# Kernel tuning notes

Hardware: AMD Instinct MI355X
Metric: run time of the kernel (lower is better)

## Reference

```python
import jax, jax.numpy as jnp
import numpy as np

EPS = 1e-5
N_HEADS = 4

def _ln(x, s, b):
    m = x.mean(-1, keepdims=True)
    v = ((x - m) ** 2).mean(-1, keepdims=True)
    return (x - m) / jnp.sqrt(v + EPS) * s + b

def _gelu(x):
    return jax.nn.gelu(x, approximate=False)  # torch nn.GELU default (erf)


def setup_inputs() -> dict:
    key = jax.random.key(0)
    ks = jax.random.split(key, 20)
    H, AF, BF, DEPTH = 256, 153, 14, 4
    n_mols, apm = 1024, 48
    n_atoms = n_mols * apm          # 49152
    max_nb = 6
    n_bonds = 3 * n_atoms           # 147456 directed bonds
    def nrm(k, shape, scale=0.02):
        return jax.random.normal(k, shape, jnp.float32) * scale
    return dict(
        f_atoms=jax.random.normal(ks[0], (n_atoms, AF), jnp.float32),
        f_bonds=jax.random.normal(ks[1], (n_bonds, BF), jnp.float32),
        a2b=jax.random.randint(ks[2], (n_atoms, max_nb), 0, n_bonds),
        b2a=jax.random.randint(ks[3], (n_bonds,), 0, n_atoms),
        b2revb=jax.random.randint(ks[4], (n_bonds,), 0, n_bonds),
        W_i=nrm(ks[5], (AF + BF, H)), b_i=jnp.zeros((H,), jnp.float32),
        W_h=nrm(ks[6], (DEPTH - 1, H, H)), b_h=jnp.zeros((DEPTH - 1, H), jnp.float32),
        ln_msg_s=jnp.ones((DEPTH - 1, H), jnp.float32), ln_msg_b=jnp.zeros((DEPTH - 1, H), jnp.float32),
        W_o=nrm(ks[7], (AF + H, H)), b_o=jnp.zeros((H,), jnp.float32),
        ln_atom_s=jnp.ones((H,), jnp.float32), ln_atom_b=jnp.zeros((H,), jnp.float32),
        q_w=nrm(ks[8], (H, H)), q_b=jnp.zeros((H,), jnp.float32),
        k_w=nrm(ks[9], (H, H)), k_b=jnp.zeros((H,), jnp.float32),
        v_w=nrm(ks[10], (H, H)), v_b=jnp.zeros((H,), jnp.float32),
        o_w=nrm(ks[11], (H, H)), o_b=jnp.zeros((H,), jnp.float32),
        ln1_s=jnp.ones((H,), jnp.float32), ln1_b=jnp.zeros((H,), jnp.float32),
        ln2_s=jnp.ones((H,), jnp.float32), ln2_b=jnp.zeros((H,), jnp.float32),
        ff1_w=nrm(ks[12], (H, 2 * H)), ff1_b=jnp.zeros((2 * H,), jnp.float32),
        ff2_w=nrm(ks[13], (2 * H, H)), ff2_b=jnp.zeros((H,), jnp.float32),
        readout_query=nrm(ks[14], (1, 1, H)),
        rk_w=nrm(ks[15], (H, H)), rk_b=jnp.zeros((H,), jnp.float32),
        n_mols=n_mols, atoms_per_mol=apm,
    )


def reference(f_atoms, f_bonds, a2b, b2a, b2revb,
              W_i, b_i, W_h, b_h, ln_msg_s, ln_msg_b, W_o, b_o,
              ln_atom_s, ln_atom_b, q_w, q_b, k_w, k_b, v_w, v_b, o_w, o_b,
              ln1_s, ln1_b, ln2_s, ln2_b, ff1_w, ff1_b, ff2_w, ff2_b,
              readout_query, rk_w, rk_b, n_mols, atoms_per_mol):
    H = W_i.shape[1]
    HD = H // N_HEADS
    depth = W_h.shape[0] + 1

    # ---- D-MPNN message passing over directed bonds ----
    message = _gelu(jnp.concatenate([f_atoms[b2a], f_bonds], axis=1) @ W_i + b_i)  # [n_bonds,H]
    for t in range(depth - 1):  # fixed small depth loop
        nei = message[a2b].sum(axis=1)                 # [n_atoms,H] gather-sum over incoming bonds
        nei_m = nei[b2a] - message[b2revb]             # [n_bonds,H] subtract reverse bond
        message = message + _gelu(_ln(nei_m, ln_msg_s[t], ln_msg_b[t]) @ W_h[t] + b_h[t])

    a_message = message[a2b].sum(axis=1)               # [n_atoms,H]
    atom_h = _gelu(jnp.concatenate([f_atoms, a_message], axis=1) @ W_o + b_o)
    atom_h = _ln(atom_h, ln_atom_s, ln_atom_b)

    # uniform scopes: padding loop becomes a reshape, mask is all-valid
    x = atom_h.reshape(n_mols, atoms_per_mol, H)

    # ---- pre-norm TransformerEncoderLayer ----
    h = _ln(x, ln1_s, ln1_b)
    def heads(t):
        return t.reshape(n_mols, atoms_per_mol, N_HEADS, HD).transpose(0, 2, 1, 3)
    q = heads(h @ q_w + q_b)
    k = heads(h @ k_w + k_b)
    v = heads(h @ v_w + v_b)
    attn = jax.nn.softmax(jnp.einsum('bhqd,bhkd->bhqk', q, k) / float(np.sqrt(HD)), axis=-1)
    ctx = jnp.einsum('bhqk,bhkd->bhqd', attn, v).transpose(0, 2, 1, 3).reshape(n_mols, atoms_per_mol, H)
    x = x + (ctx @ o_w + o_b)
    h2 = _ln(x, ln2_s, ln2_b)
    x = x + (_gelu(h2 @ ff1_w + ff1_b) @ ff2_w + ff2_b)

    # ---- attention-weighted readout ----
    keys = x @ rk_w + rk_b                             # [B,S,H]
    scores = jnp.einsum('bsh,h->bs', keys, readout_query[0, 0])
    w = jax.nn.softmax(scores, axis=-1)[..., None]
    return (x * w).sum(axis=1)                         # [B,H]
```

## Files before the change

### kernel.cpp

```cpp
#include <hip/hip_runtime.h>
#include <hip/hip_bf16.h>
#include <math.h>

#define H 256
#define AFEAT 153
#define BFEAT 14
#define KINIT 167
#define NA 49152
#define NB 147456
#define NMOL 1024
#define APM 48
#define MAXNB 6
#define NHEAD 4
#define HDIM 64
#define EPSLN 1e-5f
#define KI_PAD 192
#define KO_PAD 448

typedef unsigned short u16;
typedef __attribute__((ext_vector_type(8))) short bf16x8;
typedef __attribute__((ext_vector_type(4))) short bf16x4;
typedef __attribute__((ext_vector_type(4))) float f32x4;

__device__ __forceinline__ float gelu_f(float x) {
    float t = -1.5957691216f * x * (1.0f + 0.044715f * x * x);
    float e = __expf(t);
#if __has_builtin(__builtin_amdgcn_rcpf)
    return x * __builtin_amdgcn_rcpf(1.0f + e);
#else
    return x / (1.0f + e);
#endif
}
__device__ __forceinline__ float wave_sum(float v) {
    #pragma unroll
    for (int m = 1; m < 64; m <<= 1) v += __shfl_xor(v, m);
    return v;
}
__device__ __forceinline__ float b2f(u16 u) {
    union { unsigned u32; float f; } c; c.u32 = ((unsigned)u) << 16; return c.f;
}
__device__ __forceinline__ float blo(unsigned w) {
    union { unsigned u; float f; } c; c.u = w << 16; return c.f;
}
__device__ __forceinline__ float bhi(unsigned w) {
    union { unsigned u; float f; } c; c.u = w & 0xffff0000u; return c.f;
}
__device__ __forceinline__ u16 f2b(float f) {
    __hip_bfloat16 h = __float2bfloat16(f);
    u16 u; __builtin_memcpy(&u, &h, 2); return u;
}
__device__ __forceinline__ ushort4 f2b4(float a, float b, float c, float d) {
    ushort4 o; o.x = f2b(a); o.y = f2b(b); o.z = f2b(c); o.w = f2b(d); return o;
}
__device__ __forceinline__ void up8(uint4 u, float* v) {
    v[0]=blo(u.x); v[1]=bhi(u.x); v[2]=blo(u.y); v[3]=bhi(u.y);
    v[4]=blo(u.z); v[5]=bhi(u.z); v[6]=blo(u.w); v[7]=bhi(u.w);
}
__device__ __forceinline__ unsigned addbf2(unsigned a, unsigned b) {
    float lo = b2f((u16)(a & 0xffff)) + b2f((u16)(b & 0xffff));
    float hi = b2f((u16)(a >> 16)) + b2f((u16)(b >> 16));
    return ((unsigned)f2b(hi) << 16) | (unsigned)f2b(lo);
}
__device__ __forceinline__ uint4 addbf8(uint4 a, uint4 b) {
    uint4 r;
    r.x = addbf2(a.x, b.x); r.y = addbf2(a.y, b.y);
    r.z = addbf2(a.z, b.z); r.w = addbf2(a.w, b.w);
    return r;
}

__device__ __forceinline__ f32x4 mfma16(bf16x4 a, bf16x4 b, f32x4 c) {
#if __has_builtin(__builtin_amdgcn_mfma_f32_16x16x16bf16_1k)
    return __builtin_amdgcn_mfma_f32_16x16x16bf16_1k(a, b, c, 0, 0, 0);
#elif __has_builtin(__builtin_amdgcn_mfma_f32_16x16x16_bf16_1k)
    return __builtin_amdgcn_mfma_f32_16x16x16_bf16_1k(a, b, c, 0, 0, 0);
#elif __has_builtin(__builtin_amdgcn_mfma_f32_16x16x16_bf16)
    return __builtin_amdgcn_mfma_f32_16x16x16_bf16(a, b, c, 0, 0, 0);
#else
    f32x4 d;
    asm("v_mfma_f32_16x16x16_bf16 %0, %1, %2, %3"
        : "=&v"(d) : "v"(a), "v"(b), "v"(c));
    return d;
#endif
}

typedef const __attribute__((address_space(1))) void* gas_ptr;
typedef __attribute__((address_space(3))) void* las_ptr;
__device__ __forceinline__ void gload_lds16(const u16* g, u16* l) {
    __builtin_amdgcn_global_load_lds((gas_ptr)g, (las_ptr)l, 16, 0, 0);
}

template<bool GELU, bool ACCUM>
__global__ __launch_bounds__(256) void gemm_mfma_k(
    const u16* __restrict__ A, int Ka,
    const u16* __restrict__ Wt,
    const float* __restrict__ bias,
    u16* __restrict__ C, int Nc, int K)
{
    __shared__ __align__(16) u16 S[128 * 128];
    u16* As = S;
    u16* Bs = S + 8192;
    const int tid = threadIdx.x;
    const int w = tid >> 6, l = tid & 63;
    const int r0 = blockIdx.x * 128;
    const int cb0 = blockIdx.y * 128;
    const int wr = (w >> 1) * 64;
    const int wc = (w & 1) * 64;

    f32x4 acc[4][4];
    #pragma unroll
    for (int m = 0; m < 4; ++m)
        #pragma unroll
        for (int n = 0; n < 4; ++n) acc[m][n] = (f32x4){0.f, 0.f, 0.f, 0.f};

    const int srow = l >> 3;
    const int ssrc = ((l & 7) * 16) ^ (srow << 4);
    const int fr = l & 15;
    const int fh = l >> 4;
    const int swz = (fr & 7) << 4;

    for (int k0 = 0; k0 < K; k0 += 64) {
        #pragma unroll
        for (int i = 0; i < 4; ++i) {
            const int seg = w * 4 + i;
            gload_lds16(A + (size_t)(r0 + seg * 8 + srow) * Ka + k0 + (ssrc >> 1),
                        &As[seg * 512]);
            gload_lds16(Wt + (size_t)(cb0 + seg * 8 + srow) * Ka + k0 + (ssrc >> 1),
                        &Bs[seg * 512]);
        }
        __syncthreads();
        #pragma unroll
        for (int s = 0; s < 2; ++s) {
            const int cbyte = ((s * 64 + fh * 16) ^ swz) >> 1;
            bf16x8 af[4], bv[4];
            #pragma unroll
            for (int m = 0; m < 4; ++m)
                af[m] = *(const bf16x8*)&As[(wr + m * 16 + fr) * 64 + cbyte];
            #pragma unroll
            for (int n = 0; n < 4; ++n)
                bv[n] = *(const bf16x8*)&Bs[(wc + n * 16 + fr) * 64 + cbyte];
            #pragma unroll
            for (int m = 0; m < 4; ++m)
                #pragma unroll
                for (int n = 0; n < 4; ++n)
                    acc[m][n] = __builtin_amdgcn_mfma_f32_16x16x32_bf16(
                        af[m], bv[n], acc[m][n], 0, 0, 0);
        }
        __syncthreads();
    }

    float bvv[4];
    #pragma unroll
    for (int n = 0; n < 4; ++n) bvv[n] = bias[cb0 + wc + n * 16 + fr];
    #pragma unroll
    for (int m = 0; m < 4; ++m)
        #pragma unroll
        for (int n = 0; n < 4; ++n) {
            const int col = wc + n * 16 + fr;
            #pragma unroll
            for (int j = 0; j < 4; ++j) {
                const int row = wr + m * 16 + fh * 4 + j;
                float v = acc[m][n][j] + bvv[n];
                if (GELU) v = gelu_f(v);
                *(u16*)((char*)S + row * 256 + ((col * 2) ^ ((row & 7) << 4))) = f2b(v);
            }
        }
    __syncthreads();
    {
        const int rrow = tid >> 1;
        const int rch = (tid & 1) * 128;
        const int rswz = (rrow & 7) << 4;
        u16* gp = C + (size_t)(r0 + rrow) * Nc + cb0 + (tid & 1) * 64;
        #pragma unroll
        for (int q = 0; q < 8; ++q) {
            uint4 dv = *(const uint4*)((const char*)S + rrow * 256 + ((rch + q * 16) ^ rswz));
            if (ACCUM) {
                uint4 ov = *(const uint4*)(gp + q * 8);
                dv = addbf8(dv, ov);
            }
            *(uint4*)(gp + q * 8) = dv;
        }
    }
}

struct LGather {
    const u16* nei; const u16* msg; const int* b2a; const int* b2revb;
    __device__ __forceinline__ void load16(int row, int g, float* v) const {
        const int a = b2a[row], rv = b2revb[row];
        const uint4* np = (const uint4*)(nei + (size_t)a * H + g * 16);
        const uint4* mp = (const uint4*)(msg + (size_t)rv * H + g * 16);
        float nv[16], mv[16];
        up8(np[0], nv); up8(np[1], nv + 8);
        up8(mp[0], mv); up8(mp[1], mv + 8);
        #pragma unroll
        for (int j = 0; j < 16; ++j) v[j] = nv[j] - mv[j];
    }
};
struct LPlain {
    const u16* X;
    __device__ __forceinline__ void load16(int row, int g, float* v) const {
        const uint4* p = (const uint4*)(X + (size_t)row * H + g * 16);
        up8(p[0], v); up8(p[1], v + 8);
    }
};

template<class L, bool GELU, bool ACCUM>
__global__ __launch_bounds__(512, 4) void fln_gemm_k(
    L ld, const u16* __restrict__ Wt,
    const float* __restrict__ lns, const float* __restrict__ lnb,
    const float* __restrict__ bias,
    const u16* __restrict__ Cold,
    u16* __restrict__ C, int Nc)
{
    __shared__ __align__(16) u16 SH[64 * 256 + 2 * 256 * 32];
    u16* Alds = SH;
    u16* Bbuf0 = SH + 16384;
    u16* Bbuf1 = SH + 16384 + 8192;
    const int tid = threadIdx.x;
    const int w = tid >> 6, l = tid & 63;
    const int r0 = blockIdx.x * 64;
    const int cb0 = blockIdx.y * 256;
    const int fr = l & 15, fh = l >> 4;
    const int swzf = (fr & 7) << 4;

    uint4 oldv[4];
    if (ACCUM) {
        const u16* op = Cold + (size_t)(r0 + (tid >> 3)) * Nc + cb0 + (tid & 7) * 32;
        #pragma unroll
        for (int q = 0; q < 4; ++q) oldv[q] = *(const uint4*)(op + q * 8);
    }

    #define STAGE_B(BB, KK) do {                                               \
        _Pragma("unroll")                                                      \
        for (int j_ = 0; j_ < 2; ++j_) {                                       \
            const int seg_ = w * 2 + j_;                                       \
            const int n_ = seg_ * 16 + (l >> 2);                               \
            const int u_ = (n_ & 3) ^ ((n_ >> 2) & 3);                         \
            gload_lds16(Wt + (size_t)(cb0 + n_) * H + (KK) * 32                \
                        + (((l & 3) ^ u_) << 3), (BB) + seg_ * 512);           \
        }                                                                      \
    } while (0)
    STAGE_B(Bbuf0, 0);

    {
        const int g = l & 15;
        float4 sv[4], bb[4];
        #pragma unroll
        for (int q = 0; q < 4; ++q) {
            sv[q] = *(const float4*)(lns + g * 16 + q * 4);
            bb[q] = *(const float4*)(lnb + g * 16 + q * 4);
        }
        #pragma unroll
        for (int i = 0; i < 2; ++i) {
            const int r = w * 8 + i * 4 + (l >> 4);
            float v[16];
            ld.load16(r0 + r, g, v);
            float s = 0.f, s2 = 0.f;
            #pragma unroll
            for (int j = 0; j < 16; ++j) { s += v[j]; s2 = fmaf(v[j], v[j], s2); }
            #pragma unroll
            for (int m = 1; m < 16; m <<= 1) {
                s += __shfl_xor(s, m);
                s2 += __shfl_xor(s2, m);
            }
            const float mean = s * (1.0f / H);
            const float var = fmaxf(s2 * (1.0f / H) - mean * mean, 0.f);
            const float inv = rsqrtf(var + EPSLN);
            const int swr = (r & 7) << 4;
            #pragma unroll
            for (int q = 0; q < 4; ++q) {
                const float* sq = (const float*)&sv[q];
                const float* bq = (const float*)&bb[q];
                ushort4 o = f2b4((v[q*4+0]-mean)*inv*sq[0] + bq[0],
                                 (v[q*4+1]-mean)*inv*sq[1] + bq[1],
                                 (v[q*4+2]-mean)*inv*sq[2] + bq[2],
                                 (v[q*4+3]-mean)*inv*sq[3] + bq[3]);
                *(ushort4*)((char*)Alds + r * 512 + ((g * 32 + q * 8) ^ swr)) = o;
            }
        }
    }

    f32x4 acc[2][4];
    #pragma unroll
    for (int m = 0; m < 2; ++m)
        #pragma unroll
        for (int n = 0; n < 4; ++n) acc[m][n] = (f32x4){0.f, 0.f, 0.f, 0.f};

    const int wr = (w >> 2) * 32;
    const int wc = (w & 3) * 64;

    __syncthreads();

    #pragma unroll
    for (int kk = 0; kk < 8; ++kk) {
        if (kk < 7) STAGE_B((kk & 1) ? Bbuf0 : Bbuf1, kk + 1);
        const u16* Bb = (kk & 1) ? Bbuf1 : Bbuf0;
        bf16x8 af[2], bv[4];
        #pragma unroll
        for (int m = 0; m < 2; ++m)
            af[m] = *(const bf16x8*)((const char*)Alds + (wr + m * 16 + fr) * 512
                    + ((kk * 64 + fh * 16) ^ swzf));
        #pragma unroll
        for (int n = 0; n < 4; ++n) {
            const int nc = wc + n * 16 + fr;
            const int u = (nc & 3) ^ ((nc >> 2) & 3);
            bv[n] = *(const bf16x8*)((const char*)Bb + nc * 64 + ((fh ^ u) << 4));
        }
        #pragma unroll
        for (int m = 0; m < 2; ++m)
            #pragma unroll
            for (int n = 0; n < 4; ++n)
                acc[m][n] = __builtin_amdgcn_mfma_f32_16x16x32_bf16(
                    af[m], bv[n], acc[m][n], 0, 0, 0);
        __syncthreads();
    }
    #undef STAGE_B

    float bvv[4];
    #pragma unroll
    for (int n = 0; n < 4; ++n) bvv[n] = bias[cb0 + wc + n * 16 + fr];
    #pragma unroll
    for (int m = 0; m < 2; ++m)
        #pragma unroll
        for (int n = 0; n < 4; ++n) {
            const int col = wc + n * 16 + fr;
            #pragma unroll
            for (int j = 0; j < 4; ++j) {
                const int row = wr + m * 16 + fh * 4 + j;
                float v = acc[m][n][j] + bvv[n];
                if (GELU) v = gelu_f(v);
                *(u16*)((char*)Alds + row * 512 + ((col * 2) ^ ((row & 7) << 4))) = f2b(v);
            }
        }
    __syncthreads();
    {
        const int rrow = tid >> 3;
        const int rch = (tid & 7) * 64;
        const int rswz = (rrow & 7) << 4;
        u16* gp = C + (size_t)(r0 + rrow) * Nc + cb0 + (tid & 7) * 32;
        #pragma unroll
        for (int q = 0; q < 4; ++q) {
            uint4 dv = *(const uint4*)((const char*)Alds + rrow * 512 + ((rch + q * 16) ^ rswz));
            if (ACCUM) dv = addbf8(dv, oldv[q]);
            *(uint4*)(gp + q * 8) = dv;
        }
    }
}

__global__ __launch_bounds__(256) void wcvt_k(const float* __restrict__ W,
    u16* __restrict__ Wt, int K, int N, int Kpad)
{
    int idx = blockIdx.x * 256 + threadIdx.x;
    if (idx >= N * Kpad) return;
    int n = idx / Kpad, kp = idx - n * Kpad;
    Wt[idx] = (kp < K) ? f2b(W[(size_t)kp * N + n]) : (u16)0;
}

__global__ void biaspack_k(const float* q, const float* k, const float* v, float* dst) {
    int t = threadIdx.x;
    dst[t] = q[t]; dst[256 + t] = k[t]; dst[512 + t] = v[t];
}

__global__ __launch_bounds__(256) void ainit_k(const float* __restrict__ fa,
    const float* __restrict__ fb, const int* __restrict__ b2a, u16* __restrict__ dst)
{
    const int w = threadIdx.x >> 6, l = threadIdx.x & 63;
    const int row = blockIdx.x * 4 + w;
    const int a = b2a[row];
    const float* fsrc = fa + (size_t)a * AFEAT;
    u16* d = dst + (size_t)row * KI_PAD;
    #pragma unroll
    for (int i = 0; i < 3; ++i) {
        int c = l + i * 64;
        float v;
        if (c < AFEAT) v = fsrc[c];
        else if (c < KINIT) v = fb[(size_t)row * BFEAT + (c - AFEAT)];
        else v = 0.f;
        d[c] = f2b(v);
    }
}

__global__ __launch_bounds__(256) void acat_k(const float* __restrict__ fa,
    const u16* __restrict__ nei, u16* __restrict__ dst)
{
    const int w = threadIdx.x >> 6, l = threadIdx.x & 63;
    const int row = blockIdx.x * 4 + w;
    const float* fsrc = fa + (size_t)row * AFEAT;
    const u16* nsrc = nei + (size_t)row * H;
    u16* d = dst + (size_t)row * KO_PAD;
    #pragma unroll
    for (int i = 0; i < 7; ++i) {
        int c = l + i * 64;
        u16 v;
        if (c < AFEAT) v = f2b(fsrc[c]);
        else if (c < AFEAT + H) v = nsrc[c - AFEAT];
        else v = 0;
        d[c] = v;
    }
}

__global__ __launch_bounds__(256) void nei_sum_k(const u16* __restrict__ msg,
    const int* __restrict__ a2b, u16* __restrict__ nei)
{
    const int wave = threadIdx.x >> 6;
    const int lane = threadIdx.x & 63;
    const int atom = blockIdx.x * 4 + wave;
    float ax = 0.f, ay = 0.f, az = 0.f, aw = 0.f;
    #pragma unroll
    for (int j = 0; j < MAXNB; ++j) {
        int b = a2b[atom * MAXNB + j];
        ushort4 v = *(const ushort4*)(msg + (size_t)b * H + lane * 4);
        ax += b2f(v.x); ay += b2f(v.y); az += b2f(v.z); aw += b2f(v.w);
    }
    *(ushort4*)(nei + (size_t)atom * H + lane * 4) = f2b4(ax, ay, az, aw);
}

__global__ __launch_bounds__(256) void row_ln_k(const u16* __restrict__ in,
    u16* __restrict__ out, const float* __restrict__ s, const float* __restrict__ b)
{
    const int wave = threadIdx.x >> 6;
    const int lane = threadIdx.x & 63;
    const int row = blockIdx.x * 4 + wave;
    ushort4 u = *(const ushort4*)(in + (size_t)row * H + lane * 4);
    float vx = b2f(u.x), vy = b2f(u.y), vz = b2f(u.z), vw = b2f(u.w);
    float mean = wave_sum(vx + vy + vz + vw) * (1.0f / H);
    float dx = vx - mean, dy = vy - mean, dz = vz - mean, dw = vw - mean;
    float var = wave_sum(dx * dx + dy * dy + dz * dz + dw * dw) * (1.0f / H);
    float inv = rsqrtf(var + EPSLN);
    float4 s4 = *(const float4*)(s + lane * 4);
    float4 b4 = *(const float4*)(b + lane * 4);
    *(ushort4*)(out + (size_t)row * H + lane * 4) =
        f2b4(dx * inv * s4.x + b4.x, dy * inv * s4.y + b4.y,
             dz * inv * s4.z + b4.z, dw * inv * s4.w + b4.w);
}

#define VPAD 268
__global__ __launch_bounds__(256) void attn_mfma_k(const u16* __restrict__ qkv,
    u16* __restrict__ ctx)
{
    __shared__ u16 Vs[48][VPAD];
    const int mol = blockIdx.x;
    const int tid = threadIdx.x;
    const int w = tid >> 6;
    const int l = tid & 63;
    const int fr = l & 15;
    const int fh = l >> 4;
    const size_t qb = (size_t)mol * APM * 768;

    {
        const int r = tid >> 4;
        const int c = (tid & 15) * 16;
        #pragma unroll
        for (int i = 0; i < 3; ++i) {
            const int row = r + i * 16;
            const u16* src = qkv + qb + (size_t)row * 768 + 512 + c;
            ushort4 a0 = *(const ushort4*)(src);
            ushort4 a1 = *(const ushort4*)(src + 4);
            ushort4 a2 = *(const ushort4*)(src + 8);
            ushort4 a3 = *(const ushort4*)(src + 12);
            *(ushort4*)&Vs[row][c]      = a0;
            *(ushort4*)&Vs[row][c + 4]  = a1;
            *(ushort4*)&Vs[row][c + 8]  = a2;
            *(ushort4*)&Vs[row][c + 12] = a3;
        }
    }
    __syncthreads();

    f32x4 st[3][3];
    {
        bf16x8 kf[3][2], qf[3][2];
        #pragma unroll
        for (int t = 0; t < 3; ++t)
            #pragma unroll
            for (int ks = 0; ks < 2; ++ks) {
                const size_t rowb = qb + (size_t)(t * 16 + fr) * 768;
                kf[t][ks] = *(const bf16x8*)(qkv + rowb + 256 + w * 64 + ks * 32 + fh * 8);
                qf[t][ks] = *(const bf16x8*)(qkv + rowb +       w * 64 + ks * 32 + fh * 8);
            }
        #pragma unroll
        for (int mi = 0; mi < 3; ++mi)
            #pragma unroll
            for (int ni = 0; ni < 3; ++ni) {
                f32x4 a = (f32x4){0.f, 0.f, 0.f, 0.f};
                a = __builtin_amdgcn_mfma_f32_16x16x32_bf16(kf[mi][0], qf[ni][0], a, 0, 0, 0);
                a = __builtin_amdgcn_mfma_f32_16x16x32_bf16(kf[mi][1], qf[ni][1], a, 0, 0, 0);
                st[mi][ni] = a;
            }
    }

    float inv_sum[3];
    #pragma unroll
    for (int ni = 0; ni < 3; ++ni) {
        float m = -1e30f;
        #pragma unroll
        for (int mi = 0; mi < 3; ++mi)
            #pragma unroll
            for (int j = 0; j < 4; ++j) m = fmaxf(m, st[mi][ni][j]);
        m = fmaxf(m, __shfl_xor(m, 16));
        m = fmaxf(m, __shfl_xor(m, 32));
        float s = 0.f;
        #pragma unroll
        for (int mi = 0; mi < 3; ++mi)
            #pragma unroll
            for (int j = 0; j < 4; ++j) {
                float e = __expf((st[mi][ni][j] - m) * 0.125f);
                st[mi][ni][j] = e;
                s += e;
            }
        s += __shfl_xor(s, 16);
        s += __shfl_xor(s, 32);
        inv_sum[ni] = 1.0f / s;
    }

    bf16x4 pf[3][3];
    #pragma unroll
    for (int mi = 0; mi < 3; ++mi)
        #pragma unroll
        for (int ni = 0; ni < 3; ++ni) {
            bf16x4 p;
            p[0] = (short)f2b(st[mi][ni][0]);
            p[1] = (short)f2b(st[mi][ni][1]);
            p[2] = (short)f2b(st[mi][ni][2]);
            p[3] = (short)f2b(st[mi][ni][3]);
            pf[mi][ni] = p;
        }

    f32x4 co[4][3];
    #pragma unroll
    for (int dt = 0; dt < 4; ++dt)
        #pragma unroll
        for (int ni = 0; ni < 3; ++ni) co[dt][ni] = (f32x4){0.f, 0.f, 0.f, 0.f};
    #pragma unroll
    for (int kt = 0; kt < 3; ++kt) {
        bf16x4 vf[4];
        #pragma unroll
        for (int dt = 0; dt < 4; ++dt) {
            const int colu = w * 64 + dt * 16 + fr;
            bf16x4 t;
            #pragma unroll
            for (int e = 0; e < 4; ++e)
                t[e] = (short)Vs[kt * 16 + fh * 4 + e][colu];
            vf[dt] = t;
        }
        #pragma unroll
        for (int dt = 0; dt < 4; ++dt)
            #pragma unroll
            for (int ni = 0; ni < 3; ++ni)
                co[dt][ni] = mfma16(vf[dt], pf[kt][ni], co[dt][ni]);
    }

    #pragma unroll
    for (int ni = 0; ni < 3; ++ni) {
        const float is = inv_sum[ni];
        u16* rowp = ctx + (size_t)(mol * APM + ni * 16 + fr) * H + w * 64;
        #pragma unroll
        for (int dt = 0; dt < 4; ++dt) {
            *(ushort4*)(rowp + dt * 16 + fh * 4) =
                f2b4(co[dt][ni][0] * is, co[dt][ni][1] * is,
                     co[dt][ni][2] * is, co[dt][ni][3] * is);
        }
    }
}

__global__ __launch_bounds__(256) void readout_prep_k(const float* __restrict__ rk_w,
    const float* __restrict__ rk_b, const float* __restrict__ query, float* __restrict__ small)
{
    __shared__ float qsh[256];
    __shared__ float red[4];
    const int t = threadIdx.x;
    qsh[t] = query[t];
    __syncthreads();
    float acc = 0.f;
    #pragma unroll
    for (int c = 0; c < 256; c += 4) {
        float4 w = *(const float4*)&rk_w[(size_t)t * 256 + c];
        acc += w.x * qsh[c] + w.y * qsh[c+1] + w.z * qsh[c+2] + w.w * qsh[c+3];
    }
    small[t] = acc;
    float term = wave_sum(rk_b[t] * qsh[t]);
    if ((t & 63) == 0) red[t >> 6] = term;
    __syncthreads();
    if (t == 0) small[256] = red[0] + red[1] + red[2] + red[3];
}

__global__ __launch_bounds__(256) void readout_k(const u16* __restrict__ x,
    const float* __restrict__ small, float* __restrict__ out)
{
    __shared__ float sc[48];
    __shared__ float rvs[256];
    const int mol = blockIdx.x;
    const int t = threadIdx.x;
    const int wave = t >> 6, lane = t & 63;
    rvs[t] = small[t];
    __syncthreads();
    const float c0 = small[256];
    const size_t xb = (size_t)mol * APM * H;
    for (int i = 0; i < 12; ++i) {
        int s = wave * 12 + i;
        ushort4 xu = *(const ushort4*)(x + xb + (size_t)s * H + lane * 4);
        float dot = b2f(xu.x) * rvs[lane*4] + b2f(xu.y) * rvs[lane*4+1]
                  + b2f(xu.z) * rvs[lane*4+2] + b2f(xu.w) * rvs[lane*4+3];
        dot = wave_sum(dot);
        if (lane == 0) sc[s] = dot + c0;
    }
    __syncthreads();
    if (wave == 0) {
        float v = (lane < 48) ? sc[lane] : -1e30f;
        float mx = v;
        #pragma unroll
        for (int m = 1; m < 64; m <<= 1) mx = fmaxf(mx, __shfl_xor(mx, m));
        float e = (lane < 48) ? __expf(v - mx) : 0.f;
        float sum = wave_sum(e);
        if (lane < 48) sc[lane] = e / sum;
    }
    __syncthreads();
    float acc = 0.f;
    for (int s = 0; s < 48; ++s) acc += sc[s] * b2f(x[xb + (size_t)s * H + t]);
    out[(size_t)mol * H + t] = acc;
}

__global__ void diag_k(float* out, int n, float val) {
    int i = blockIdx.x * 256 + threadIdx.x;
    if (i < n) out[i] = (i == 0) ? val : 0.f;
}

extern "C" void kernel_launch(void* const* d_in, const int* in_sizes, int n_in,
                              void* d_out, int out_size, void* d_ws, size_t ws_size,
                              hipStream_t stream)
{
    const float* f_atoms = (const float*)d_in[0];
    const float* f_bonds = (const float*)d_in[1];
    const int*   a2b     = (const int*)d_in[2];
    const int*   b2a     = (const int*)d_in[3];
    const int*   b2revb  = (const int*)d_in[4];
    const float* W_i = (const float*)d_in[5];
    const float* b_i = (const float*)d_in[6];
    const float* W_h = (const float*)d_in[7];
    const float* b_h = (const float*)d_in[8];
    const float* ln_msg_s = (const float*)d_in[9];
    const float* ln_msg_b = (const float*)d_in[10];
    const float* W_o = (const float*)d_in[11];
    const float* b_o = (const float*)d_in[12];
    const float* ln_atom_s = (const float*)d_in[13];
    const float* ln_atom_b = (const float*)d_in[14];
    const float* q_w = (const float*)d_in[15];
    const float* q_b = (const float*)d_in[16];
    const float* k_w = (const float*)d_in[17];
    const float* k_b = (const float*)d_in[18];
    const float* v_w = (const float*)d_in[19];
    const float* v_b = (const float*)d_in[20];
    const float* o_w = (const float*)d_in[21];
    const float* o_b = (const float*)d_in[22];
    const float* ln1_s = (const float*)d_in[23];
    const float* ln1_b = (const float*)d_in[24];
    const float* ln2_s = (const float*)d_in[25];
    const float* ln2_b = (const float*)d_in[26];
    const float* ff1_w = (const float*)d_in[27];
    const float* ff1_b = (const float*)d_in[28];
    const float* ff2_w = (const float*)d_in[29];
    const float* ff2_b = (const float*)d_in[30];
    const float* rquery = (const float*)d_in[31];
    const float* rk_w = (const float*)d_in[32];
    const float* rk_b = (const float*)d_in[33];

    const size_t SZ_MSG = (size_t)NB * H;
    const size_t SZ_NEI = (size_t)NA * H;
    const size_t W_I_SZ  = 256 * KI_PAD;
    const size_t W_H_SZ  = 3 * 256 * 256;
    const size_t W_O_SZ  = 256 * KO_PAD;
    const size_t W_QKV_SZ = 768 * 256;
    const size_t W_OG_SZ = 256 * 256;
    const size_t W_F1_SZ = 512 * 256;
    const size_t W_F2_SZ = 256 * 512;
    const size_t wtotal = W_I_SZ + W_H_SZ + W_O_SZ + W_QKV_SZ + W_OG_SZ + W_F1_SZ + W_F2_SZ;
    const size_t required = (2 * SZ_MSG + SZ_NEI + wtotal) * 2 + 768 * 4 + 257 * 4 + 256;
    if (ws_size < required) {
        diag_k<<<dim3((out_size + 255) / 256), dim3(256), 0, stream>>>(
            (float*)d_out, out_size, (float)(ws_size >> 20));
        return;
    }

    u16* msgA   = (u16*)d_ws;
    u16* msgB   = msgA + SZ_MSG;
    u16* nei    = msgB + SZ_MSG;
    u16* wt_i   = nei + SZ_NEI;
    u16* wt_h   = wt_i + W_I_SZ;
    u16* wt_o   = wt_h + W_H_SZ;
    u16* wt_qkv = wt_o + W_O_SZ;
    u16* wt_og  = wt_qkv + W_QKV_SZ;
    u16* wt_f1  = wt_og + W_OG_SZ;
    u16* wt_f2  = wt_f1 + W_F1_SZ;
    float* qkvb = (float*)(wt_f2 + W_F2_SZ);
    float* small = qkvb + 768;
    float* out = (float*)d_out;

    dim3 blk(256);
    dim3 blk5(512);
    #define WCVT(W, DST, K, N, KP) wcvt_k<<<dim3(((N)*(KP)+255)/256), blk, 0, stream>>>(W, DST, K, N, KP)

    WCVT(W_i, wt_i, KINIT, 256, KI_PAD);
    WCVT(W_h,           wt_h,           256, 256, 256);
    WCVT(W_h + 65536,   wt_h + 65536,   256, 256, 256);
    WCVT(W_h + 131072,  wt_h + 131072,  256, 256, 256);
    WCVT(W_o, wt_o, AFEAT + H, 256, KO_PAD);
    WCVT(q_w, wt_qkv,          256, 256, 256);
    WCVT(k_w, wt_qkv + 65536,  256, 256, 256);
    WCVT(v_w, wt_qkv + 131072, 256, 256, 256);
    WCVT(o_w, wt_og, 256, 256, 256);
    WCVT(ff1_w, wt_f1, 256, 512, 256);
    WCVT(ff2_w, wt_f2, 512, 256, 512);
    biaspack_k<<<dim3(1), blk, 0, stream>>>(q_b, k_b, v_b, qkvb);

    ainit_k<<<dim3(NB / 4), blk, 0, stream>>>(f_atoms, f_bonds, b2a, msgB);
    gemm_mfma_k<true, false><<<dim3(NB / 128, 2), blk, 0, stream>>>(
        msgB, KI_PAD, wt_i, b_i, msgA, H, KI_PAD);

    u16* cur = msgA;
    u16* oth = msgB;
    for (int t = 0; t < 3; ++t) {
        nei_sum_k<<<dim3(NA / 4), blk, 0, stream>>>(cur, a2b, nei);
        fln_gemm_k<LGather, true, true><<<dim3(NB / 64, 1), blk5, 0, stream>>>(
            LGather{nei, cur, b2a, b2revb}, wt_h + (size_t)t * 65536,
            ln_msg_s + t * H, ln_msg_b + t * H, b_h + t * H,
            cur, oth, H);
        u16* tmp = cur; cur = oth; oth = tmp;
    }

    nei_sum_k<<<dim3(NA / 4), blk, 0, stream>>>(cur, a2b, nei);
    acat_k<<<dim3(NA / 4), blk, 0, stream>>>(f_atoms, nei, oth);
    u16* x = cur;
    gemm_mfma_k<true, false><<<dim3(NA / 128, 2), blk, 0, stream>>>(
        oth, KO_PAD, wt_o, b_o, x, H, KO_PAD);
    row_ln_k<<<dim3(NA / 4), blk, 0, stream>>>(x, x, ln_atom_s, ln_atom_b);

    u16* qkv = oth;
    fln_gemm_k<LPlain, false, false><<<dim3(NA / 64, 3), blk5, 0, stream>>>(
        LPlain{x}, wt_qkv, ln1_s, ln1_b, qkvb, x, qkv, 768);
    u16* ctx = nei;
    attn_mfma_k<<<dim3(NMOL), blk, 0, stream>>>(qkv, ctx);
    gemm_mfma_k<false, true><<<dim3(NA / 128, 2), blk, 0, stream>>>(
        ctx, H, wt_og, o_b, x, H, H);
    u16* ff1o = oth;
    fln_gemm_k<LPlain, true, false><<<dim3(NA / 64, 2), blk5, 0, stream>>>(
        LPlain{x}, wt_f1, ln2_s, ln2_b, ff1_b, x, ff1o, 512);
    gemm_mfma_k<false, true><<<dim3(NA / 128, 2), blk, 0, stream>>>(
        ff1o, 512, wt_f2, ff2_b, x, H, 512);

    readout_prep_k<<<dim3(1), blk, 0, stream>>>(rk_w, rk_b, rquery, small);
    readout_k<<<dim3(NMOL), blk, 0, stream>>>(x, small, out);
}
```

Measured before the change: 734.5 us.

## Fuse init feature gather into GEMM and restructure fused GEMM B staging

Drops the separate ainit kernel and its padded intermediate by adding an LInit loader that gathers atom and bond features straight into the GEMM A tile, with the LayerNorm prologue made optional. The fused GEMM now stages B in 128-column halves, with 16 smaller stages and a smaller LDS footprint, and raises wave priority around the MFMAs. The output-projection GEMM is moved onto this kernel. The exact-reciprocal GELU replaces the rcp builtin. The feature gather reads scalar fp32 values uncoalesced, and W_i is now padded to 256 in K, which adds zero MFMA work.

```diff
diff --git a/kernel.cpp b/kernel.cpp
--- a/kernel.cpp
+++ b/kernel.cpp
@@ -14,7 +14,6 @@
 #define NHEAD 4
 #define HDIM 64
 #define EPSLN 1e-5f
-#define KI_PAD 192
 #define KO_PAD 448
 
 typedef unsigned short u16;
@@ -25,11 +24,7 @@
 __device__ __forceinline__ float gelu_f(float x) {
     float t = -1.5957691216f * x * (1.0f + 0.044715f * x * x);
     float e = __expf(t);
-#if __has_builtin(__builtin_amdgcn_rcpf)
-    return x * __builtin_amdgcn_rcpf(1.0f + e);
-#else
     return x / (1.0f + e);
-#endif
 }
 __device__ __forceinline__ float wave_sum(float v) {
     #pragma unroll
@@ -202,25 +197,42 @@
         up8(p[0], v); up8(p[1], v + 8);
     }
 };
-
-template<class L, bool GELU, bool ACCUM>
-__global__ __launch_bounds__(512, 4) void fln_gemm_k(
+struct LInit {
+    const float* fa; const float* fb; const int* b2a;
+    __device__ __forceinline__ void load16(int row, int g, float* v) const {
+        const int a = b2a[row];
+        const int c0 = g * 16;
+        #pragma unroll
+        for (int j = 0; j < 16; ++j) {
+            const int c = c0 + j;
+            float x = 0.f;
+            if (c < AFEAT) x = fa[(size_t)a * AFEAT + c];
+            else if (c < KINIT) x = fb[(size_t)row * BFEAT + (c - AFEAT)];
+            v[j] = x;
+        }
+    }
+};
+
+template<class L, bool DOLN, bool GELU, bool ACCUM>
+__global__ __launch_bounds__(512, 4) void fgemm_k(
     L ld, const u16* __restrict__ Wt,
     const float* __restrict__ lns, const float* __restrict__ lnb,
     const float* __restrict__ bias,
     const u16* __restrict__ Cold,
     u16* __restrict__ C, int Nc)
 {
-    __shared__ __align__(16) u16 SH[64 * 256 + 2 * 256 * 32];
+    __shared__ __align__(16) u16 SH[64 * 256 + 2 * 128 * 32];
     u16* Alds = SH;
-    u16* Bbuf0 = SH + 16384;
-    u16* Bbuf1 = SH + 16384 + 8192;
+    u16* Bb0 = SH + 16384;
+    u16* Bb1 = SH + 16384 + 4096;
     const int tid = threadIdx.x;
     const int w = tid >> 6, l = tid & 63;
     const int r0 = blockIdx.x * 64;
     const int cb0 = blockIdx.y * 256;
     const int fr = l & 15, fh = l >> 4;
     const int swzf = (fr & 7) << 4;
+    const int brow = w * 16 + (l >> 2);
+    const int bsl  = ((l & 3) ^ (brow & 3)) * 8;
 
     uint4 oldv[4];
     if (ACCUM) {
@@ -229,108 +241,106 @@
         for (int q = 0; q < 4; ++q) oldv[q] = *(const uint4*)(op + q * 8);
     }
 
-    #define STAGE_B(BB, KK) do {                                               \
-        _Pragma("unroll")                                                      \
-        for (int j_ = 0; j_ < 2; ++j_) {                                       \
-            const int seg_ = w * 2 + j_;                                       \
-            const int n_ = seg_ * 16 + (l >> 2);                               \
-            const int u_ = (n_ & 3) ^ ((n_ >> 2) & 3);                         \
-            gload_lds16(Wt + (size_t)(cb0 + n_) * H + (KK) * 32                \
-                        + (((l & 3) ^ u_) << 3), (BB) + seg_ * 512);           \
-        }                                                                      \
-    } while (0)
-    STAGE_B(Bbuf0, 0);
+    #define STAGE(S, BB) \
+        gload_lds16(Wt + (size_t)(cb0 + ((S) >> 3) * 128 + brow) * 256 + ((S) & 7) * 32 + bsl, \
+                    (BB) + w * 512)
+
+    STAGE(0, Bb0);
 
     {
         const int g = l & 15;
-        float4 sv[4], bb[4];
-        #pragma unroll
-        for (int q = 0; q < 4; ++q) {
-            sv[q] = *(const float4*)(lns + g * 16 + q * 4);
-            bb[q] = *(const float4*)(lnb + g * 16 + q * 4);
-        }
         #pragma unroll
         for (int i = 0; i < 2; ++i) {
             const int r = w * 8 + i * 4 + (l >> 4);
             float v[16];
             ld.load16(r0 + r, g, v);
-            float s = 0.f, s2 = 0.f;
-            #pragma unroll
-            for (int j = 0; j < 16; ++j) { s += v[j]; s2 = fmaf(v[j], v[j], s2); }
-            #pragma unroll
-            for (int m = 1; m < 16; m <<= 1) {
-                s += __shfl_xor(s, m);
-                s2 += __shfl_xor(s2, m);
+            if (DOLN) {
+                float s = 0.f, s2 = 0.f;
+                #pragma unroll
+                for (int j = 0; j < 16; ++j) { s += v[j]; s2 = fmaf(v[j], v[j], s2); }
+                #pragma unroll
+                for (int m = 1; m < 16; m <<= 1) {
+                    s += __shfl_xor(s, m);
+                    s2 += __shfl_xor(s2, m);
+                }
+                const float mean = s * (1.0f / H);
+                const float var = fmaxf(s2 * (1.0f / H) - mean * mean, 0.f);
+                const float inv = rsqrtf(var + EPSLN);
+                #pragma unroll
+                for (int j = 0; j < 16; ++j)
+                    v[j] = (v[j] - mean) * inv * lns[g * 16 + j] + lnb[g * 16 + j];
             }
-            const float mean = s * (1.0f / H);
-            const float var = fmaxf(s2 * (1.0f / H) - mean * mean, 0.f);
-            const float inv = rsqrtf(var + EPSLN);
             const int swr = (r & 7) << 4;
-            #pragma unroll
-            for (int q = 0; q < 4; ++q) {
-                const float* sq = (const float*)&sv[q];
-                const float* bq = (const float*)&bb[q];
-                ushort4 o = f2b4((v[q*4+0]-mean)*inv*sq[0] + bq[0],
-                                 (v[q*4+1]-mean)*inv*sq[1] + bq[1],
-                                 (v[q*4+2]-mean)*inv*sq[2] + bq[2],
-                                 (v[q*4+3]-mean)*inv*sq[3] + bq[3]);
-                *(ushort4*)((char*)Alds + r * 512 + ((g * 32 + q * 8) ^ swr)) = o;
+            u16 o8[8];
+            #pragma unroll
+            for (int j = 0; j < 8; ++j) o8[j] = f2b(v[j]);
+            *(uint4*)((char*)Alds + r * 512 + ((g * 16) ^ swr)) = *(uint4*)o8;
+            #pragma unroll
+            for (int j = 0; j < 8; ++j) o8[j] = f2b(v[8 + j]);
+            *(uint4*)((char*)Alds + r * 512 + 256 + ((g * 16) ^ swr)) = *(uint4*)o8;
+        }
+    }
+
+    f32x4 acc[2][2][2];
+    #pragma unroll
+    for (int p = 0; p < 2; ++p)
+        #pragma unroll
+        for (int m = 0; m < 2; ++m)
+            #pragma unroll
+            for (int n = 0; n < 2; ++n) acc[p][m][n] = (f32x4){0.f, 0.f, 0.f, 0.f};
+
+    const int wr = (w >> 2) * 32;
+    const int wc = (w & 3) * 32;
+
+    __syncthreads();
+
+    #pragma unroll
+    for (int s = 0; s < 16; ++s) {
+        if (s < 15) {
+            if (s & 1) STAGE(s + 1, Bb0); else STAGE(s + 1, Bb1);
+        }
+        const u16* Bb = (s & 1) ? Bb1 : Bb0;
+        const int ph = s >> 3, kk = s & 7;
+        bf16x8 af[2], bv[2];
+        #pragma unroll
+        for (int m = 0; m < 2; ++m) {
+            const int c = kk * 4 + fh;
+            af[m] = *(const bf16x8*)((const char*)Alds + (wr + m * 16 + fr) * 512
+                     + ((((c & 1) << 8) | ((c >> 1) << 4)) ^ swzf));
+        }
+        #pragma unroll
+        for (int n = 0; n < 2; ++n) {
+            const int nc = wc + n * 16 + fr;
+            bv[n] = *(const bf16x8*)((const char*)Bb + nc * 64 + ((fh ^ (nc & 3)) << 4));
+        }
+        __builtin_amdgcn_s_setprio(1);
+        #pragma unroll
+        for (int m = 0; m < 2; ++m)
+            #pragma unroll
+            for (int n = 0; n < 2; ++n)
+                acc[ph][m][n] = __builtin_amdgcn_mfma_f32_16x16x32_bf16(
+                    af[m], bv[n], acc[ph][m][n], 0, 0, 0);
+        __builtin_amdgcn_s_setprio(0);
+        __syncthreads();
+    }
+    #undef STAGE
+
+    #pragma unroll
+    for (int ph = 0; ph < 2; ++ph)
+        #pragma unroll
+        for (int m = 0; m < 2; ++m)
+            #pragma unroll
+            for (int n = 0; n < 2; ++n) {
+                const int col = ph * 128 + wc + n * 16 + fr;
+                const float bv_ = bias[cb0 + col];
+                #pragma unroll
+                for (int j = 0; j < 4; ++j) {
+                    const int row = wr + m * 16 + fh * 4 + j;
+                    float v = acc[ph][m][n][j] + bv_;
+                    if (GELU) v = gelu_f(v);
+                    *(u16*)((char*)Alds + row * 512 + ((col * 2) ^ ((row & 7) << 4))) = f2b(v);
+                }
             }
-        }
-    }
-
-    f32x4 acc[2][4];
-    #pragma unroll
-    for (int m = 0; m < 2; ++m)
-        #pragma unroll
-        for (int n = 0; n < 4; ++n) acc[m][n] = (f32x4){0.f, 0.f, 0.f, 0.f};
-
-    const int wr = (w >> 2) * 32;
-    const int wc = (w & 3) * 64;
-
-    __syncthreads();
-
-    #pragma unroll
-    for (int kk = 0; kk < 8; ++kk) {
-        if (kk < 7) STAGE_B((kk & 1) ? Bbuf0 : Bbuf1, kk + 1);
-        const u16* Bb = (kk & 1) ? Bbuf1 : Bbuf0;
-        bf16x8 af[2], bv[4];
-        #pragma unroll
-        for (int m = 0; m < 2; ++m)
-            af[m] = *(const bf16x8*)((const char*)Alds + (wr + m * 16 + fr) * 512
-                    + ((kk * 64 + fh * 16) ^ swzf));
-        #pragma unroll
-        for (int n = 0; n < 4; ++n) {
-            const int nc = wc + n * 16 + fr;
-            const int u = (nc & 3) ^ ((nc >> 2) & 3);
-            bv[n] = *(const bf16x8*)((const char*)Bb + nc * 64 + ((fh ^ u) << 4));
-        }
-        #pragma unroll
-        for (int m = 0; m < 2; ++m)
-            #pragma unroll
-            for (int n = 0; n < 4; ++n)
-                acc[m][n] = __builtin_amdgcn_mfma_f32_16x16x32_bf16(
-                    af[m], bv[n], acc[m][n], 0, 0, 0);
-        __syncthreads();
-    }
-    #undef STAGE_B
-
-    float bvv[4];
-    #pragma unroll
-    for (int n = 0; n < 4; ++n) bvv[n] = bias[cb0 + wc + n * 16 + fr];
-    #pragma unroll
-    for (int m = 0; m < 2; ++m)
-        #pragma unroll
-        for (int n = 0; n < 4; ++n) {
-            const int col = wc + n * 16 + fr;
-            #pragma unroll
-            for (int j = 0; j < 4; ++j) {
-                const int row = wr + m * 16 + fh * 4 + j;
-                float v = acc[m][n][j] + bvv[n];
-                if (GELU) v = gelu_f(v);
-                *(u16*)((char*)Alds + row * 512 + ((col * 2) ^ ((row & 7) << 4))) = f2b(v);
-            }
-        }
     __syncthreads();
     {
         const int rrow = tid >> 3;
@@ -358,25 +368,6 @@
 __global__ void biaspack_k(const float* q, const float* k, const float* v, float* dst) {
     int t = threadIdx.x;
     dst[t] = q[t]; dst[256 + t] = k[t]; dst[512 + t] = v[t];
-}
-
-__global__ __launch_bounds__(256) void ainit_k(const float* __restrict__ fa,
-    const float* __restrict__ fb, const int* __restrict__ b2a, u16* __restrict__ dst)
-{
-    const int w = threadIdx.x >> 6, l = threadIdx.x & 63;
-    const int row = blockIdx.x * 4 + w;
-    const int a = b2a[row];
-    const float* fsrc = fa + (size_t)a * AFEAT;
-    u16* d = dst + (size_t)row * KI_PAD;
-    #pragma unroll
-    for (int i = 0; i < 3; ++i) {
-        int c = l + i * 64;
-        float v;
-        if (c < AFEAT) v = fsrc[c];
-        else if (c < KINIT) v = fb[(size_t)row * BFEAT + (c - AFEAT)];
-        else v = 0.f;
-        d[c] = f2b(v);
-    }
 }
 
 __global__ __launch_bounds__(256) void acat_k(const float* __restrict__ fa,
@@ -664,7 +655,7 @@
 
     const size_t SZ_MSG = (size_t)NB * H;
     const size_t SZ_NEI = (size_t)NA * H;
-    const size_t W_I_SZ  = 256 * KI_PAD;
+    const size_t W_I_SZ  = 256 * 256;
     const size_t W_H_SZ  = 3 * 256 * 256;
     const size_t W_O_SZ  = 256 * KO_PAD;
     const size_t W_QKV_SZ = 768 * 256;
@@ -697,7 +688,7 @@
     dim3 blk5(512);
     #define WCVT(W, DST, K, N, KP) wcvt_k<<<dim3(((N)*(KP)+255)/256), blk, 0, stream>>>(W, DST, K, N, KP)
 
-    WCVT(W_i, wt_i, KINIT, 256, KI_PAD);
+    WCVT(W_i, wt_i, KINIT, 256, 256);
     WCVT(W_h,           wt_h,           256, 256, 256);
     WCVT(W_h + 65536,   wt_h + 65536,   256, 256, 256);
     WCVT(W_h + 131072,  wt_h + 131072,  256, 256, 256);
@@ -710,15 +701,14 @@
     WCVT(ff2_w, wt_f2, 512, 256, 512);
     biaspack_k<<<dim3(1), blk, 0, stream>>>(q_b, k_b, v_b, qkvb);
 
-    ainit_k<<<dim3(NB / 4), blk, 0, stream>>>(f_atoms, f_bonds, b2a, msgB);
-    gemm_mfma_k<true, false><<<dim3(NB / 128, 2), blk, 0, stream>>>(
-        msgB, KI_PAD, wt_i, b_i, msgA, H, KI_PAD);
+    fgemm_k<LInit, false, true, false><<<dim3(NB / 64, 1), blk5, 0, stream>>>(
+        LInit{f_atoms, f_bonds, b2a}, wt_i, nullptr, nullptr, b_i, msgA, msgA, H);
 
     u16* cur = msgA;
     u16* oth = msgB;
     for (int t = 0; t < 3; ++t) {
         nei_sum_k<<<dim3(NA / 4), blk, 0, stream>>>(cur, a2b, nei);
-        fln_gemm_k<LGather, true, true><<<dim3(NB / 64, 1), blk5, 0, stream>>>(
+        fgemm_k<LGather, true, true, true><<<dim3(NB / 64, 1), blk5, 0, stream>>>(
             LGather{nei, cur, b2a, b2revb}, wt_h + (size_t)t * 65536,
             ln_msg_s + t * H, ln_msg_b + t * H, b_h + t * H,
             cur, oth, H);
@@ -733,14 +723,14 @@
     row_ln_k<<<dim3(NA / 4), blk, 0, stream>>>(x, x, ln_atom_s, ln_atom_b);
 
     u16* qkv = oth;
-    fln_gemm_k<LPlain, false, false><<<dim3(NA / 64, 3), blk5, 0, stream>>>(
+    fgemm_k<LPlain, true, false, false><<<dim3(NA / 64, 3), blk5, 0, stream>>>(
         LPlain{x}, wt_qkv, ln1_s, ln1_b, qkvb, x, qkv, 768);
     u16* ctx = nei;
     attn_mfma_k<<<dim3(NMOL), blk, 0, stream>>>(qkv, ctx);
-    gemm_mfma_k<false, true><<<dim3(NA / 128, 2), blk, 0, stream>>>(
-        ctx, H, wt_og, o_b, x, H, H);
+    fgemm_k<LPlain, false, false, true><<<dim3(NA / 64, 1), blk5, 0, stream>>>(
+        LPlain{ctx}, wt_og, nullptr, nullptr, o_b, x, x, H);
     u16* ff1o = oth;
-    fln_gemm_k<LPlain, true, false><<<dim3(NA / 64, 2), blk5, 0, stream>>>(
+    fgemm_k<LPlain, true, true, false><<<dim3(NA / 64, 2), blk5, 0, stream>>>(
         LPlain{x}, wt_f1, ln2_s, ln2_b, ff1_b, x, ff1o, 512);
     gemm_mfma_k<false, true><<<dim3(NA / 128, 2), blk, 0, stream>>>(
         ff1o, 512, wt_f2, ff2_b, x, H, 512);
```

New measurement: 792.8 us. 1.08x slower.

## Loop over output column tiles inside fused LN-GEMM to reuse normalized A tile

Applied to the files above, without the earlier changes.

The fused layernorm+GEMM kernel now keeps its normalized 64-row A tile in LDS and loops over all output column tiles (NT) in one block, instead of launching one block per column tile and recomputing the gather/LN each time. It also remaps block IDs for locality, changes the A LDS layout, adds s_setprio around the MFMA sequence, and swaps the GELU reciprocal intrinsic for a true division. This removes redundant row loads and LN work for the QKV and FF1 projections, but it makes each block serial over tiles, adds extra barriers, and reduces the number of blocks per launch.

```diff
diff --git a/kernel.cpp b/kernel.cpp
--- a/kernel.cpp
+++ b/kernel.cpp
@@ -25,11 +25,7 @@
 __device__ __forceinline__ float gelu_f(float x) {
     float t = -1.5957691216f * x * (1.0f + 0.044715f * x * x);
     float e = __expf(t);
-#if __has_builtin(__builtin_amdgcn_rcpf)
-    return x * __builtin_amdgcn_rcpf(1.0f + e);
-#else
     return x / (1.0f + e);
-#endif
 }
 __device__ __forceinline__ float wave_sum(float v) {
     #pragma unroll
@@ -203,7 +199,7 @@
     }
 };
 
-template<class L, bool GELU, bool ACCUM>
+template<class L, bool DOLN, bool GELU, bool ACCUM, int NT>
 __global__ __launch_bounds__(512, 4) void fln_gemm_k(
     L ld, const u16* __restrict__ Wt,
     const float* __restrict__ lns, const float* __restrict__ lnb,
@@ -213,77 +209,69 @@
 {
     __shared__ __align__(16) u16 SH[64 * 256 + 2 * 256 * 32];
     u16* Alds = SH;
-    u16* Bbuf0 = SH + 16384;
-    u16* Bbuf1 = SH + 16384 + 8192;
+    u16* Bb0 = SH + 16384;
+    u16* Bb1 = SH + 16384 + 8192;
+    u16* E   = SH + 16384;
     const int tid = threadIdx.x;
     const int w = tid >> 6, l = tid & 63;
-    const int r0 = blockIdx.x * 64;
-    const int cb0 = blockIdx.y * 256;
+    const int bid = blockIdx.x;
+    const int sb = (bid & 7) * ((int)gridDim.x >> 3) + (bid >> 3);
+    const int r0 = sb * 64;
     const int fr = l & 15, fh = l >> 4;
     const int swzf = (fr & 7) << 4;
 
     uint4 oldv[4];
     if (ACCUM) {
-        const u16* op = Cold + (size_t)(r0 + (tid >> 3)) * Nc + cb0 + (tid & 7) * 32;
+        const u16* op = Cold + (size_t)(r0 + (tid >> 3)) * Nc + (tid & 7) * 32;
         #pragma unroll
         for (int q = 0; q < 4; ++q) oldv[q] = *(const uint4*)(op + q * 8);
     }
 
-    #define STAGE_B(BB, KK) do {                                               \
+    #define STAGE(CT, KK, BB) do {                                             \
         _Pragma("unroll")                                                      \
         for (int j_ = 0; j_ < 2; ++j_) {                                       \
             const int seg_ = w * 2 + j_;                                       \
             const int n_ = seg_ * 16 + (l >> 2);                               \
             const int u_ = (n_ & 3) ^ ((n_ >> 2) & 3);                         \
-            gload_lds16(Wt + (size_t)(cb0 + n_) * H + (KK) * 32                \
+            gload_lds16(Wt + (size_t)((CT) + n_) * H + (KK) * 32               \
                         + (((l & 3) ^ u_) << 3), (BB) + seg_ * 512);           \
         }                                                                      \
     } while (0)
-    STAGE_B(Bbuf0, 0);
+    STAGE(0, 0, Bb0);
 
     {
         const int g = l & 15;
-        float4 sv[4], bb[4];
-        #pragma unroll
-        for (int q = 0; q < 4; ++q) {
-            sv[q] = *(const float4*)(lns + g * 16 + q * 4);
-            bb[q] = *(const float4*)(lnb + g * 16 + q * 4);
-        }
         #pragma unroll
         for (int i = 0; i < 2; ++i) {
             const int r = w * 8 + i * 4 + (l >> 4);
             float v[16];
             ld.load16(r0 + r, g, v);
-            float s = 0.f, s2 = 0.f;
-            #pragma unroll
-            for (int j = 0; j < 16; ++j) { s += v[j]; s2 = fmaf(v[j], v[j], s2); }
-            #pragma unroll
-            for (int m = 1; m < 16; m <<= 1) {
-                s += __shfl_xor(s, m);
-                s2 += __shfl_xor(s2, m);
-            }
-            const float mean = s * (1.0f / H);
-            const float var = fmaxf(s2 * (1.0f / H) - mean * mean, 0.f);
-            const float inv = rsqrtf(var + EPSLN);
+            if (DOLN) {
+                float s = 0.f, s2 = 0.f;
+                #pragma unroll
+                for (int j = 0; j < 16; ++j) { s += v[j]; s2 = fmaf(v[j], v[j], s2); }
+                #pragma unroll
+                for (int m = 1; m < 16; m <<= 1) {
+                    s += __shfl_xor(s, m);
+                    s2 += __shfl_xor(s2, m);
+                }
+                const float mean = s * (1.0f / H);
+                const float var = fmaxf(s2 * (1.0f / H) - mean * mean, 0.f);
+                const float inv = rsqrtf(var + EPSLN);
+                #pragma unroll
+                for (int j = 0; j < 16; ++j)
+                    v[j] = (v[j] - mean) * inv * lns[g * 16 + j] + lnb[g * 16 + j];
+            }
             const int swr = (r & 7) << 4;
-            #pragma unroll
-            for (int q = 0; q < 4; ++q) {
-                const float* sq = (const float*)&sv[q];
-                const float* bq = (const float*)&bb[q];
-                ushort4 o = f2b4((v[q*4+0]-mean)*inv*sq[0] + bq[0],
-                                 (v[q*4+1]-mean)*inv*sq[1] + bq[1],
-                                 (v[q*4+2]-mean)*inv*sq[2] + bq[2],
-                                 (v[q*4+3]-mean)*inv*sq[3] + bq[3]);
-                *(ushort4*)((char*)Alds + r * 512 + ((g * 32 + q * 8) ^ swr)) = o;
-            }
-        }
-    }
-
-    f32x4 acc[2][4];
-    #pragma unroll
-    for (int m = 0; m < 2; ++m)
-        #pragma unroll
-        for (int n = 0; n < 4; ++n) acc[m][n] = (f32x4){0.f, 0.f, 0.f, 0.f};
+            u16 o8[8];
+            #pragma unroll
+            for (int j = 0; j < 8; ++j) o8[j] = f2b(v[j]);
+            *(uint4*)((char*)Alds + r * 512 + ((g * 16) ^ swr)) = *(uint4*)o8;
+            #pragma unroll
+            for (int j = 0; j < 8; ++j) o8[j] = f2b(v[8 + j]);
+            *(uint4*)((char*)Alds + r * 512 + 256 + ((g * 16) ^ swr)) = *(uint4*)o8;
+        }
+    }
 
     const int wr = (w >> 2) * 32;
     const int wc = (w & 3) * 64;
@@ -291,59 +279,74 @@
     __syncthreads();
 
     #pragma unroll
-    for (int kk = 0; kk < 8; ++kk) {
-        if (kk < 7) STAGE_B((kk & 1) ? Bbuf0 : Bbuf1, kk + 1);
-        const u16* Bb = (kk & 1) ? Bbuf1 : Bbuf0;
-        bf16x8 af[2], bv[4];
+    for (int t = 0; t < NT; ++t) {
+        const int ct = t * 256;
+        if (t > 0) {
+            STAGE(ct, 0, Bb0);
+            __syncthreads();
+        }
+        f32x4 acc[2][4];
         #pragma unroll
         for (int m = 0; m < 2; ++m)
-            af[m] = *(const bf16x8*)((const char*)Alds + (wr + m * 16 + fr) * 512
-                    + ((kk * 64 + fh * 16) ^ swzf));
-        #pragma unroll
-        for (int n = 0; n < 4; ++n) {
-            const int nc = wc + n * 16 + fr;
-            const int u = (nc & 3) ^ ((nc >> 2) & 3);
-            bv[n] = *(const bf16x8*)((const char*)Bb + nc * 64 + ((fh ^ u) << 4));
-        }
+            #pragma unroll
+            for (int n = 0; n < 4; ++n) acc[m][n] = (f32x4){0.f, 0.f, 0.f, 0.f};
+
+        #pragma unroll
+        for (int kk = 0; kk < 8; ++kk) {
+            if (kk < 7) STAGE(ct, kk + 1, (kk & 1) ? Bb0 : Bb1);
+            const u16* Bb = (kk & 1) ? Bb1 : Bb0;
+            bf16x8 af[2], bv[4];
+            #pragma unroll
+            for (int m = 0; m < 2; ++m)
+                af[m] = *(const bf16x8*)((const char*)Alds + (wr + m * 16 + fr) * 512
+                         + ((fh & 1) << 8) + (((kk * 2 + (fh >> 1)) << 4) ^ swzf));
+            #pragma unroll
+            for (int n = 0; n < 4; ++n) {
+                const int nc = wc + n * 16 + fr;
+                const int u = (nc & 3) ^ ((nc >> 2) & 3);
+                bv[n] = *(const bf16x8*)((const char*)Bb + nc * 64 + ((fh ^ u) << 4));
+            }
+            __builtin_amdgcn_s_setprio(1);
+            #pragma unroll
+            for (int m = 0; m < 2; ++m)
+                #pragma unroll
+                for (int n = 0; n < 4; ++n)
+                    acc[m][n] = __builtin_amdgcn_mfma_f32_16x16x32_bf16(
+                        af[m], bv[n], acc[m][n], 0, 0, 0);
+            __builtin_amdgcn_s_setprio(0);
+            __syncthreads();
+        }
+
         #pragma unroll
         for (int m = 0; m < 2; ++m)
             #pragma unroll
-            for (int n = 0; n < 4; ++n)
-                acc[m][n] = __builtin_amdgcn_mfma_f32_16x16x32_bf16(
-                    af[m], bv[n], acc[m][n], 0, 0, 0);
+            for (int n = 0; n < 4; ++n) {
+                const int col = wc + n * 16 + fr;
+                const float bv_ = bias[ct + col];
+                #pragma unroll
+                for (int j = 0; j < 4; ++j) {
+                    const int row = wr + m * 16 + fh * 4 + j;
+                    float v = acc[m][n][j] + bv_;
+                    if (GELU) v = gelu_f(v);
+                    *(u16*)((char*)E + row * 512 + ((col * 2) ^ ((row & 7) << 4))) = f2b(v);
+                }
+            }
         __syncthreads();
-    }
-    #undef STAGE_B
-
-    float bvv[4];
-    #pragma unroll
-    for (int n = 0; n < 4; ++n) bvv[n] = bias[cb0 + wc + n * 16 + fr];
-    #pragma unroll
-    for (int m = 0; m < 2; ++m)
-        #pragma unroll
-        for (int n = 0; n < 4; ++n) {
-            const int col = wc + n * 16 + fr;
-            #pragma unroll
-            for (int j = 0; j < 4; ++j) {
-                const int row = wr + m * 16 + fh * 4 + j;
-                float v = acc[m][n][j] + bvv[n];
-                if (GELU) v = gelu_f(v);
-                *(u16*)((char*)Alds + row * 512 + ((col * 2) ^ ((row & 7) << 4))) = f2b(v);
-            }
-        }
-    __syncthreads();
-    {
-        const int rrow = tid >> 3;
-        const int rch = (tid & 7) * 64;
-        const int rswz = (rrow & 7) << 4;
-        u16* gp = C + (size_t)(r0 + rrow) * Nc + cb0 + (tid & 7) * 32;
-        #pragma unroll
-        for (int q = 0; q < 4; ++q) {
-            uint4 dv = *(const uint4*)((const char*)Alds + rrow * 512 + ((rch + q * 16) ^ rswz));
-            if (ACCUM) dv = addbf8(dv, oldv[q]);
-            *(uint4*)(gp + q * 8) = dv;
-        }
-    }
+        {
+            const int rrow = tid >> 3;
+            const int rch = (tid & 7) * 64;
+            const int rswz = (rrow & 7) << 4;
+            u16* gp = C + (size_t)(r0 + rrow) * Nc + ct + (tid & 7) * 32;
+            #pragma unroll
+            for (int q = 0; q < 4; ++q) {
+                uint4 dv = *(const uint4*)((const char*)E + rrow * 512 + ((rch + q * 16) ^ rswz));
+                if (ACCUM) dv = addbf8(dv, oldv[q]);
+                *(uint4*)(gp + q * 8) = dv;
+            }
+        }
+        if (t + 1 < NT) __syncthreads();
+    }
+    #undef STAGE
 }
 
 __global__ __launch_bounds__(256) void wcvt_k(const float* __restrict__ W,
@@ -718,7 +721,7 @@
     u16* oth = msgB;
     for (int t = 0; t < 3; ++t) {
         nei_sum_k<<<dim3(NA / 4), blk, 0, stream>>>(cur, a2b, nei);
-        fln_gemm_k<LGather, true, true><<<dim3(NB / 64, 1), blk5, 0, stream>>>(
+        fln_gemm_k<LGather, true, true, true, 1><<<dim3(NB / 64), blk5, 0, stream>>>(
             LGather{nei, cur, b2a, b2revb}, wt_h + (size_t)t * 65536,
             ln_msg_s + t * H, ln_msg_b + t * H, b_h + t * H,
             cur, oth, H);
@@ -733,14 +736,14 @@
     row_ln_k<<<dim3(NA / 4), blk, 0, stream>>>(x, x, ln_atom_s, ln_atom_b);
 
     u16* qkv = oth;
-    fln_gemm_k<LPlain, false, false><<<dim3(NA / 64, 3), blk5, 0, stream>>>(
+    fln_gemm_k<LPlain, true, false, false, 3><<<dim3(NA / 64), blk5, 0, stream>>>(
         LPlain{x}, wt_qkv, ln1_s, ln1_b, qkvb, x, qkv, 768);
     u16* ctx = nei;
     attn_mfma_k<<<dim3(NMOL), blk, 0, stream>>>(qkv, ctx);
     gemm_mfma_k<false, true><<<dim3(NA / 128, 2), blk, 0, stream>>>(
         ctx, H, wt_og, o_b, x, H, H);
     u16* ff1o = oth;
-    fln_gemm_k<LPlain, true, false><<<dim3(NA / 64, 2), blk5, 0, stream>>>(
+    fln_gemm_k<LPlain, true, true, false, 2><<<dim3(NA / 64), blk5, 0, stream>>>(
         LPlain{x}, wt_f1, ln2_s, ln2_b, ff1_b, x, ff1o, 512);
     gemm_mfma_k<false, true><<<dim3(NA / 128, 2), blk, 0, stream>>>(
         ff1o, 512, wt_f2, ff2_b, x, H, 512);
```

Measured after the change: 826.7 us. 1.13x slower.
